# Performance work log

Measured on AMD Instinct MI355X. Metric: run time of the kernel, lower is better.

## Reference

```python
import jax, jax.numpy as jnp
import numpy as np

# Config matching init_kwargs
C, H_IMG, W_IMG = 3, 224, 224
N_PATCHES = 14
PS = H_IMG // N_PATCHES            # 16
INPUT_D = C * PS * PS              # 768
HID = 768
N_HEADS = 12
DH = HID // N_HEADS                # 64
N_BLOCKS = 12
MLP_RATIO = 4
SEQ = N_PATCHES * N_PATCHES + 1    # 197
EPS = 1e-5


def _pos_embed():
    # sin on even dims, cos on odd dims, exponent uses (j - j%2)/d  (faithful to loop)
    i = jnp.arange(SEQ, dtype=jnp.float32)[:, None]
    j = jnp.arange(HID, dtype=jnp.float32)[None, :]
    expo = (j - jnp.mod(j, 2.0)) / HID
    ang = i / jnp.power(10000.0, expo)
    return jnp.where(jnp.mod(jnp.arange(HID), 2) == 0, jnp.sin(ang), jnp.cos(ang))


def setup_inputs() -> dict:
    key = jax.random.key(0)
    ks = jax.random.split(key, 16)
    s = 0.02
    d_ff = MLP_RATIO * HID
    inp = {
        'images': jax.random.normal(ks[0], (16, C, H_IMG, W_IMG), dtype=jnp.float32),
        'w_map': jax.random.normal(ks[1], (HID, INPUT_D), dtype=jnp.float32) * s,
        'b_map': jnp.zeros((HID,), dtype=jnp.float32),
        'class_token': jax.random.uniform(ks[2], (1, HID), dtype=jnp.float32),
        'pos_embed': _pos_embed(),
        'qw': jax.random.normal(ks[3], (N_BLOCKS, N_HEADS, DH, DH), dtype=jnp.float32) * s,
        'qb': jnp.zeros((N_BLOCKS, N_HEADS, DH), dtype=jnp.float32),
        'kw': jax.random.normal(ks[4], (N_BLOCKS, N_HEADS, DH, DH), dtype=jnp.float32) * s,
        'kb': jnp.zeros((N_BLOCKS, N_HEADS, DH), dtype=jnp.float32),
        'vw': jax.random.normal(ks[5], (N_BLOCKS, N_HEADS, DH, DH), dtype=jnp.float32) * s,
        'vb': jnp.zeros((N_BLOCKS, N_HEADS, DH), dtype=jnp.float32),
        'ln1_w': jnp.ones((N_BLOCKS, HID), dtype=jnp.float32),
        'ln1_b': jnp.zeros((N_BLOCKS, HID), dtype=jnp.float32),
        'ln2_w': jnp.ones((N_BLOCKS, HID), dtype=jnp.float32),
        'ln2_b': jnp.zeros((N_BLOCKS, HID), dtype=jnp.float32),
        'mlp_w1': jax.random.normal(ks[6], (N_BLOCKS, d_ff, HID), dtype=jnp.float32) * s,
        'mlp_b1': jnp.zeros((N_BLOCKS, d_ff), dtype=jnp.float32),
        'mlp_w2': jax.random.normal(ks[7], (N_BLOCKS, HID, d_ff), dtype=jnp.float32) * s,
        'mlp_b2': jnp.zeros((N_BLOCKS, HID), dtype=jnp.float32),
    }
    return inp


def _layernorm(x, w, b):
    mu = jnp.mean(x, axis=-1, keepdims=True)
    var = jnp.mean(jnp.square(x - mu), axis=-1, keepdims=True)
    return (x - mu) * jax.lax.rsqrt(var + EPS) * w + b


def _patchify(images):
    # [N,C,H,W] -> [N, np^2, C*ps*ps]; per-patch flatten order is (c, ph, pw)
    n = images.shape[0]
    x = images.reshape(n, C, N_PATCHES, PS, N_PATCHES, PS)
    x = x.transpose(0, 2, 4, 1, 3, 5)  # n, pi, pj, c, ph, pw
    return x.reshape(n, N_PATCHES * N_PATCHES, INPUT_D)


def _msa(x, qw, qb, kw, kb, vw, vb):
    # x: [B,S,D]; per-head Linear on head slices; torch Linear: y = x @ W.T + b
    b_, s_, _ = x.shape
    xh = x.reshape(b_, s_, N_HEADS, DH)
    q = jnp.einsum('bshd,hod->bsho', xh, qw) + qb
    k = jnp.einsum('bshd,hod->bsho', xh, kw) + kb
    v = jnp.einsum('bshd,hod->bsho', xh, vw) + vb
    attn = jax.nn.softmax(jnp.einsum('bsho,btho->bhst', q, k) / (DH ** 0.5), axis=-1)
    out = jnp.einsum('bhst,btho->bsho', attn, v)
    return out.reshape(b_, s_, HID)


def reference(images, w_map, b_map, class_token, pos_embed, qw, qb, kw, kb, vw, vb,
              ln1_w, ln1_b, ln2_w, ln2_b, mlp_w1, mlp_b1, mlp_w2, mlp_b2):
    patches = _patchify(images)                       # [N, 196, 768]
    tokens = patches @ w_map.T + b_map                # [N, 196, HID]
    n = tokens.shape[0]
    cls = jnp.broadcast_to(class_token[None], (n, 1, HID))
    out = jnp.concatenate([cls, tokens], axis=1) + pos_embed[None]  # [N, SEQ, HID]
    for l in range(N_BLOCKS):
        out = out + _msa(_layernorm(out, ln1_w[l], ln1_b[l]),
                         qw[l], qb[l], kw[l], kb[l], vw[l], vb[l])
        h = _layernorm(out, ln2_w[l], ln2_b[l])
        h = jax.nn.gelu(h @ mlp_w1[l].T + mlp_b1[l], approximate=False)
        out = out + (h @ mlp_w2[l].T + mlp_b2[l])
    return out
```

## Files before the change

kernel.cpp:

```cpp
#include <hip/hip_runtime.h>
#include <hip/hip_bf16.h>
#include <math.h>

typedef __attribute__((ext_vector_type(4))) float f32x4;
typedef __attribute__((ext_vector_type(8))) __bf16 bf16x8;
typedef __attribute__((ext_vector_type(8))) short short8;
typedef __attribute__((ext_vector_type(4))) unsigned short us4;
typedef __attribute__((ext_vector_type(8))) unsigned short us8;

#define B_    16
#define SEQ_  197
#define TOK_  3152
#define HID_  768
#define MPAD_ 3200
#define NP_   3136
#define DFF_  3072
#define PSZ_  (MPAD_ * HID_)
#define QKVP_ 14336
#define BHN_  192

__device__ __forceinline__ unsigned short f2bf(float x) {
  union { float f; unsigned int u; } v; v.f = x;
  unsigned int r = v.u + 0x7fffu + ((v.u >> 16) & 1u);
  return (unsigned short)(r >> 16);
}

__device__ __forceinline__ float bf2f(unsigned short u) {
  union { unsigned int i; float f; } v; v.i = ((unsigned int)u) << 16; return v.f;
}

__device__ __forceinline__ f32x4 mfma16(bf16x8 a, bf16x8 b, f32x4 c) {
  return __builtin_amdgcn_mfma_f32_16x16x32_bf16(a, b, c, 0, 0, 0);
}

__device__ __forceinline__ void cp16(const void* g, void* l) {
  __builtin_amdgcn_global_load_lds((__attribute__((address_space(1))) void*)(g),
                                   (__attribute__((address_space(3))) void*)(l),
                                   16, 0, 0);
}

__device__ __forceinline__ float gelu_f(float x) {
  float y = x * (1.5957691216f + 0.0713548162f * x * x);
  float e = __expf(y);
  float r = 1.0f / (1.0f + e);
  return x - x * r;
}

__device__ __forceinline__ void conv8(const float* __restrict__ s, unsigned short* __restrict__ d, int c) {
  const float* sp = s + (size_t)c * 8;
  f32x4 v0 = *(const f32x4*)sp;
  f32x4 v1 = *(const f32x4*)(sp + 4);
  us8 o;
  o[0] = f2bf(v0[0]); o[1] = f2bf(v0[1]); o[2] = f2bf(v0[2]); o[3] = f2bf(v0[3]);
  o[4] = f2bf(v1[0]); o[5] = f2bf(v1[1]); o[6] = f2bf(v1[2]); o[7] = f2bf(v1[3]);
  *(us8*)(d + (size_t)c * 8) = o;
}

__global__ __launch_bounds__(256) void patchcls_kernel(const float* __restrict__ img,
                                                       unsigned short* __restrict__ Pb,
                                                       const float* __restrict__ ct,
                                                       const float* __restrict__ pos,
                                                       float* __restrict__ X,
                                                       const float* __restrict__ wmap,
                                                       unsigned short* __restrict__ Wmb,
                                                       const float* __restrict__ cw1,
                                                       unsigned short* __restrict__ cd1,
                                                       const float* __restrict__ cw2,
                                                       unsigned short* __restrict__ cd2) {
  int bid = blockIdx.x;
  if (bid >= 2736) {
    int bb = bid - 2736;
    const float* s; unsigned short* d;
    if (bb < 1152) { s = cw1; d = cd1; } else { s = cw2; d = cd2; bb -= 1152; }
    conv8(s, d, bb * 256 + threadIdx.x);
    return;
  }
  if (bid >= 2448) {
    int c = (bid - 2448) * 256 + threadIdx.x;
    conv8(wmap, Wmb, c);
    return;
  }
  if (bid >= 2400) {
    int j = (bid - 2400) * 256 + threadIdx.x;
    if (j < B_ * HID_) {
      int b = j / HID_, t = j - b * HID_;
      X[(size_t)b * SEQ_ * HID_ + t] = ct[t] + pos[t];
    }
    return;
  }
  int gid = bid * 256 + threadIdx.x;
  int m = gid / 192;
  int j4 = (gid - m * 192) * 4;
  us4 o;
  if (m < NP_) {
    int n = m / 196, p = m - n * 196;
    int pi = p / 14, pj = p - pi * 14;
    int c = j4 >> 8, rem = j4 & 255, ph = rem >> 4, pw = rem & 15;
    const float* src = img + (((size_t)(n * 3 + c) * 224 + pi * 16 + ph) * 224 + pj * 16 + pw);
    f32x4 v = *(const f32x4*)src;
    o[0] = f2bf(v[0]); o[1] = f2bf(v[1]); o[2] = f2bf(v[2]); o[3] = f2bf(v[3]);
  } else {
    o[0] = 0; o[1] = 0; o[2] = 0; o[3] = 0;
  }
  *(us4*)(Pb + (size_t)m * HID_ + j4) = o;
}

__global__ __launch_bounds__(256) void convw_kernel(const float* __restrict__ s1, unsigned short* __restrict__ d1,
                                                    const float* __restrict__ s2, unsigned short* __restrict__ d2,
                                                    int nchunks) {
  int half = gridDim.x >> 1;
  int b = blockIdx.x;
  const float* s; unsigned short* d;
  if (b < half) { s = s1; d = d1; } else { s = s2; d = d2; b -= half; }
  int c = b * 256 + threadIdx.x;
  if (c >= nchunks) return;
  conv8(s, d, c);
}

__global__ __launch_bounds__(256) void gemm_embed(const unsigned short* __restrict__ A,
                                                  const unsigned short* __restrict__ Bw,
                                                  const float* __restrict__ bias,
                                                  const float* __restrict__ pos,
                                                  float* __restrict__ Xout) {
  constexpr int MI = 2, NJ = 2, BM = 64, BN = 64;
  __shared__ unsigned short As[BM * 64];
  __shared__ unsigned short Bs[BN * 64];
  const int tid = threadIdx.x;
  const int w = tid >> 6, lane = tid & 63;
  const int lr = lane & 15, kg = lane >> 4;
  int bid = blockIdx.x;
  int cpx = gridDim.x >> 3;
  int swz = (bid & 7) * cpx + (bid >> 3);
  const int by = swz / 12, bx = swz - by * 12;
  const int m0 = by * BM, n0 = bx * BN;
  const int wr = w >> 1, wc = w & 1;
  const f32x4 z4 = {0.f, 0.f, 0.f, 0.f};
  f32x4 acc[MI][NJ];
#pragma unroll
  for (int i = 0; i < MI; ++i)
#pragma unroll
    for (int j = 0; j < NJ; ++j) acc[i][j] = z4;
  for (int k0 = 0; k0 < 768; k0 += 64) {
#pragma unroll
    for (int is = 0; is < MI; ++is) {
      int chunk = is * 256 + tid;
      int row = chunk >> 3, cc = (chunk & 7) * 8;
      cp16(A + (size_t)(m0 + row) * 768 + k0 + cc, As + is * 2048 + w * 512);
    }
#pragma unroll
    for (int is = 0; is < NJ; ++is) {
      int chunk = is * 256 + tid;
      int row = chunk >> 3, cc = (chunk & 7) * 8;
      cp16(Bw + (size_t)(n0 + row) * 768 + k0 + cc, Bs + is * 2048 + w * 512);
    }
    __syncthreads();
#pragma unroll
    for (int kk = 0; kk < 64; kk += 32) {
      bf16x8 af[MI], bfr[NJ];
#pragma unroll
      for (int i = 0; i < MI; ++i)
        af[i] = *(const bf16x8*)&As[(wr * (BM / 2) + i * 16 + lr) * 64 + kk + kg * 8];
#pragma unroll
      for (int j = 0; j < NJ; ++j)
        bfr[j] = *(const bf16x8*)&Bs[(wc * (BN / 2) + j * 16 + lr) * 64 + kk + kg * 8];
#pragma unroll
      for (int i = 0; i < MI; ++i)
#pragma unroll
        for (int j = 0; j < NJ; ++j)
          acc[i][j] = mfma16(af[i], bfr[j], acc[i][j]);
    }
    __syncthreads();
  }
#pragma unroll
  for (int i = 0; i < MI; ++i) {
    int mbase = m0 + wr * (BM / 2) + i * 16 + kg * 4;
#pragma unroll
    for (int j = 0; j < NJ; ++j) {
      int col = n0 + wc * (BN / 2) + j * 16 + lr;
#pragma unroll
      for (int qr = 0; qr < 4; ++qr) {
        int m = mbase + qr;
        if (m < NP_) {
          int nimg = m / 196;
          int tok = m + nimg + 1;
          int prow = m - nimg * 196 + 1;
          Xout[(size_t)tok * HID_ + col] = acc[i][j][qr] + bias[col] + pos[(size_t)prow * HID_ + col];
        }
      }
    }
  }
}

template<int EPI, int NT>
__global__ __launch_bounds__(512, 2) void gemm4b(const unsigned short* __restrict__ A,
                                                 const unsigned short* __restrict__ Bw,
                                                 int ldk, int gx, int gy,
                                                 const float* __restrict__ bias,
                                                 unsigned short* __restrict__ Pout,
                                                 unsigned short* __restrict__ Hout) {
  __shared__ unsigned short lds4[32768];
  const int tid = threadIdx.x;
  const int wid = tid >> 6, lane = tid & 63;
  const int lr = lane & 15, kg = lane >> 4;
  const int wm = wid >> 2, wn = wid & 3;
  const int nwg = gridDim.x;
  const int q = nwg >> 3, r = nwg & 7;
  const int xcd = blockIdx.x & 7, idx = blockIdx.x >> 3;
  const int wgid = (xcd < r ? xcd * (q + 1) : r * (q + 1) + (xcd - r) * q) + idx;
  const int bx = wgid % gx;
  const int rest = wgid / gx;
  const int by = rest % gy;
  const int z = rest / gy;
  const int m0 = by * 128, n0 = bx * 128;
  const unsigned short* Abase = A + (size_t)m0 * ldk + z * (NT * 32);
  const unsigned short* Bbase = Bw + (size_t)n0 * ldk + z * (NT * 32);

  const int ra = tid >> 2, ua = tid & 3;
  const int sk = (ua ^ ((ra >> 1) & 3)) * 8;
  const int wbase = wid * 512;

#pragma unroll
  for (int t = 0; t < 3; ++t) {
    unsigned short* lb = lds4 + t * 8192;
    cp16(Abase + (size_t)ra * ldk + sk + t * 32, lb + wbase);
    cp16(Bbase + (size_t)ra * ldk + sk + t * 32, lb + 4096 + wbase);
  }

  int offA[4], offB[2];
#pragma unroll
  for (int i = 0; i < 4; ++i) {
    int rr = wm * 64 + i * 16 + lr;
    offA[i] = rr * 32 + ((kg ^ ((rr >> 1) & 3)) * 8);
  }
#pragma unroll
  for (int j = 0; j < 2; ++j) {
    int rr = wn * 32 + j * 16 + lr;
    offB[j] = rr * 32 + ((kg ^ ((rr >> 1) & 3)) * 8);
  }

  const f32x4 z4 = {0.f, 0.f, 0.f, 0.f};
  f32x4 acc[4][2];
#pragma unroll
  for (int i = 0; i < 4; ++i)
#pragma unroll
    for (int j = 0; j < 2; ++j) acc[i][j] = z4;

#pragma unroll 1
  for (int k = 0; k < NT; ++k) {
    asm volatile("s_waitcnt vmcnt(4)" ::: "memory");
    __builtin_amdgcn_s_barrier();
    __builtin_amdgcn_sched_barrier(0);
    const unsigned short* lp = lds4 + (k & 3) * 8192;
    const int tn = k + 3;
    const int ts = (tn >= NT) ? tn - NT : tn;
    unsigned short* tb = lds4 + (tn & 3) * 8192;
    bf16x8 af[4], bfr[2];
#pragma unroll
    for (int i = 0; i < 4; ++i)
      af[i] = *(const bf16x8*)(lp + offA[i]);
#pragma unroll
    for (int j = 0; j < 2; ++j)
      bfr[j] = *(const bf16x8*)(lp + 4096 + offB[j]);
    cp16(Abase + (size_t)ra * ldk + sk + ts * 32, tb + wbase);
    cp16(Bbase + (size_t)ra * ldk + sk + ts * 32, tb + 4096 + wbase);
    __builtin_amdgcn_s_barrier();
    __builtin_amdgcn_s_setprio(1);
#pragma unroll
    for (int i = 0; i < 4; ++i)
#pragma unroll
      for (int j = 0; j < 2; ++j) acc[i][j] = mfma16(af[i], bfr[j], acc[i][j]);
    __builtin_amdgcn_s_setprio(0);
  }

#pragma unroll
  for (int i = 0; i < 4; ++i) {
    int mbase = m0 + wm * 64 + i * 16 + kg * 4;
#pragma unroll
    for (int j = 0; j < 2; ++j) {
      int col = n0 + wn * 32 + j * 16 + lr;
      float bv = (EPI == 1) ? bias[col] : 0.f;
#pragma unroll
      for (int qr = 0; qr < 4; ++qr) {
        int m = mbase + qr;
        if (m < TOK_) {
          float v = acc[i][j][qr];
          if (EPI == 1) {
            Hout[(size_t)m * 3072 + col] = f2bf(gelu_f(v + bv));
          } else {
            Pout[(size_t)z * PSZ_ + (size_t)m * 768 + col] = f2bf(v);
          }
        }
      }
    }
  }
}

template<int MODE>
__global__ __launch_bounds__(256) void ln_kernel(float* __restrict__ X,
                                                 const unsigned short* __restrict__ P, const float* __restrict__ pb,
                                                 const float* __restrict__ gw, const float* __restrict__ gb,
                                                 unsigned short* __restrict__ Y,
                                                 const float* __restrict__ cw1, unsigned short* __restrict__ cd1,
                                                 const float* __restrict__ cw2, unsigned short* __restrict__ cd2) {
  int bb = (int)blockIdx.x - 800;
  if (bb >= 0) {
    const float* s; unsigned short* d;
    if (bb < 1152) { s = cw1; d = cd1; } else { s = cw2; d = cd2; bb -= 1152; }
    conv8(s, d, bb * 256 + threadIdx.x);
    return;
  }
  int row = blockIdx.x * 4 + (threadIdx.x >> 6);
  int lane = threadIdx.x & 63;
  if (row >= MPAD_) return;
  size_t base = (size_t)row * HID_;
  if (row >= TOK_) {
    us4 zz; zz[0] = 0; zz[1] = 0; zz[2] = 0; zz[3] = 0;
#pragma unroll
    for (int i = 0; i < 3; ++i) *(us4*)(Y + base + i * 256 + lane * 4) = zz;
    return;
  }
  f32x4 xv[3];
  float s1 = 0.f, s2 = 0.f;
#pragma unroll
  for (int i = 0; i < 3; ++i) {
    int cb = i * 256 + lane * 4;
    f32x4 v = *(const f32x4*)(X + base + cb);
    if (MODE == 2) {
      const unsigned short* pp = P + base + cb;
      us4 p0 = *(const us4*)(pp);
      us4 p1 = *(const us4*)(pp + PSZ_);
      us4 p2 = *(const us4*)(pp + 2 * (size_t)PSZ_);
      us4 p3 = *(const us4*)(pp + 3 * (size_t)PSZ_);
      f32x4 bb2 = *(const f32x4*)(pb + cb);
#pragma unroll
      for (int e = 0; e < 4; ++e)
        v[e] += bf2f(p0[e]) + bf2f(p1[e]) + bf2f(p2[e]) + bf2f(p3[e]) + bb2[e];
      *(f32x4*)(X + base + cb) = v;
    }
    xv[i] = v;
    s1 += v[0] + v[1] + v[2] + v[3];
    s2 += v[0] * v[0] + v[1] * v[1] + v[2] * v[2] + v[3] * v[3];
  }
#pragma unroll
  for (int d = 1; d < 64; d <<= 1) {
    s1 += __shfl_xor(s1, d);
    s2 += __shfl_xor(s2, d);
  }
  float mu = s1 * (1.f / 768.f);
  float var = s2 * (1.f / 768.f) - mu * mu;
  float rs = rsqrtf(var + 1e-5f);
#pragma unroll
  for (int i = 0; i < 3; ++i) {
    int cb = i * 256 + lane * 4;
    us4 o;
#pragma unroll
    for (int e = 0; e < 4; ++e)
      o[e] = f2bf((xv[i][e] - mu) * rs * gw[cb + e] + gb[cb + e]);
    *(us4*)(Y + base + cb) = o;
  }
}

__global__ __launch_bounds__(256) void redfin_kernel(float* __restrict__ X, const unsigned short* __restrict__ P,
                                                     const float* __restrict__ b2) {
  int i = blockIdx.x * 256 + threadIdx.x;
  if (i >= TOK_ * 192) return;
  int m = i / 192, c4 = (i - m * 192) * 4;
  size_t off = (size_t)m * HID_ + c4;
  f32x4 v = *(const f32x4*)(X + off);
  const unsigned short* pp = P + off;
  us4 p0 = *(const us4*)(pp);
  us4 p1 = *(const us4*)(pp + PSZ_);
  us4 p2 = *(const us4*)(pp + 2 * (size_t)PSZ_);
  us4 p3 = *(const us4*)(pp + 3 * (size_t)PSZ_);
  f32x4 bb = *(const f32x4*)(b2 + c4);
#pragma unroll
  for (int e = 0; e < 4; ++e)
    v[e] += bf2f(p0[e]) + bf2f(p1[e]) + bf2f(p2[e]) + bf2f(p3[e]) + bb[e];
  *(f32x4*)(X + off) = v;
}

__device__ __forceinline__ void loadw_frags(const float* __restrict__ W, int lr, int kg, bf16x8* wf) {
#pragma unroll
  for (int j = 0; j < 4; ++j)
#pragma unroll
    for (int kk = 0; kk < 2; ++kk) {
      const float* wp = W + (j * 16 + lr) * 64 + kk * 32 + kg * 8;
      f32x4 w0 = *(const f32x4*)wp;
      f32x4 w1 = *(const f32x4*)(wp + 4);
      short8 t;
      t[0] = (short)f2bf(w0[0]); t[1] = (short)f2bf(w0[1]); t[2] = (short)f2bf(w0[2]); t[3] = (short)f2bf(w0[3]);
      t[4] = (short)f2bf(w1[0]); t[5] = (short)f2bf(w1[1]); t[6] = (short)f2bf(w1[2]); t[7] = (short)f2bf(w1[3]);
      wf[j * 2 + kk] = __builtin_bit_cast(bf16x8, t);
    }
}

__global__ __launch_bounds__(128) void qkvproj_kernel(const unsigned short* __restrict__ Y,
                                                      const float* __restrict__ qw, const float* __restrict__ qb,
                                                      const float* __restrict__ kw, const float* __restrict__ kb,
                                                      const float* __restrict__ vw, const float* __restrict__ vb,
                                                      unsigned short* __restrict__ Qo,
                                                      unsigned short* __restrict__ Ko,
                                                      unsigned short* __restrict__ Vto) {
  const int blk = blockIdx.x;
  const int half = blk & 1;
  const int bp = blk >> 1;
  const int p = bp % 3, bh = bp / 3;
  const int b = bh / 12, h = bh - b * 12;
  const int wv = threadIdx.x >> 6, lane = threadIdx.x & 63;
  const int lr = lane & 15, kg = lane >> 4;
  const int ws = half * 2 + wv;
  const float* W; const float* bs; unsigned short* out;
  if (p == 0)      { W = qw + h * 4096; bs = qb + h * 64; out = Qo; }
  else if (p == 1) { W = kw + h * 4096; bs = kb + h * 64; out = Ko; }
  else             { W = vw + h * 4096; bs = vb + h * 64; out = Vto; }
  const float scale = (p == 0) ? 0.125f : 1.0f;
  bf16x8 wf[8];
  loadw_frags(W, lr, kg, wf);
  float bj[4];
#pragma unroll
  for (int j = 0; j < 4; ++j) bj[j] = bs[j * 16 + lr];
  out += (size_t)bh * QKVP_;
  const f32x4 z4 = {0.f, 0.f, 0.f, 0.f};
  const short8 zs = {0, 0, 0, 0, 0, 0, 0, 0};
#pragma unroll
  for (int i = 0; i < 4; ++i) {
    int t = ws + 4 * i;
    if (t < 14) {
      int s = t * 16 + lr;
      bf16x8 a0 = __builtin_bit_cast(bf16x8, zs), a1 = a0;
      if (s < SEQ_) {
        const unsigned short* yp = Y + (size_t)(b * SEQ_ + s) * HID_ + h * 64 + kg * 8;
        a0 = *(const bf16x8*)yp;
        a1 = *(const bf16x8*)(yp + 32);
      }
      f32x4 acc[4] = {z4, z4, z4, z4};
#pragma unroll
      for (int j = 0; j < 4; ++j) {
        acc[j] = mfma16(a0, wf[j * 2 + 0], acc[j]);
        acc[j] = mfma16(a1, wf[j * 2 + 1], acc[j]);
      }
      if (p == 2) {
#pragma unroll
        for (int j = 0; j < 4; ++j) {
          us4 pk;
#pragma unroll
          for (int qr = 0; qr < 4; ++qr) {
            int srow = t * 16 + kg * 4 + qr;
            pk[qr] = (srow < SEQ_) ? f2bf(acc[j][qr] + bj[j]) : (unsigned short)0;
          }
          *(us4*)&out[(j * 16 + lr) * 224 + t * 16 + kg * 4] = pk;
        }
      } else {
#pragma unroll
        for (int j = 0; j < 4; ++j)
#pragma unroll
          for (int qr = 0; qr < 4; ++qr) {
            int row = t * 16 + kg * 4 + qr;
            out[row * 64 + j * 16 + lr] = f2bf((acc[j][qr] + bj[j]) * scale);
          }
      }
    }
  }
}

__global__ __launch_bounds__(64) void attn_kernel(const unsigned short* __restrict__ Qb,
                                                  const unsigned short* __restrict__ Kb,
                                                  const unsigned short* __restrict__ Vtb,
                                                  float* __restrict__ X) {
  __shared__ unsigned short plds[16 * 232];
  const int blk = blockIdx.x;
  const int qt = blk % 13, bh = blk / 13;
  const int b = bh / 12, h = bh - b * 12;
  const int lane = threadIdx.x;
  const int lr = lane & 15, kg = lane >> 4;
  const f32x4 z4 = {0.f, 0.f, 0.f, 0.f};
  const unsigned short* Qp = Qb + (size_t)bh * QKVP_;
  const unsigned short* Kp = Kb + (size_t)bh * QKVP_;
  const unsigned short* Vp = Vtb + (size_t)bh * QKVP_;
  {
    int rr = lane >> 2, c0 = 208 + (lane & 3) * 4;
    us4 zz; zz[0] = 0; zz[1] = 0; zz[2] = 0; zz[3] = 0;
    *(us4*)&plds[rr * 232 + c0] = zz;
  }
  bf16x8 aq0 = *(const bf16x8*)&Qp[(qt * 16 + lr) * 64 + kg * 8];
  bf16x8 aq1 = *(const bf16x8*)&Qp[(qt * 16 + lr) * 64 + 32 + kg * 8];
  f32x4 s[13];
#pragma unroll
  for (int nt = 0; nt < 13; ++nt) {
    const unsigned short* kp = Kp + (nt * 16 + lr) * 64 + kg * 8;
    bf16x8 b0 = *(const bf16x8*)kp;
    bf16x8 b1 = *(const bf16x8*)(kp + 32);
    f32x4 acc = mfma16(aq0, b0, z4);
    s[nt] = mfma16(aq1, b1, acc);
  }
#pragma unroll
  for (int qr = 0; qr < 4; ++qr) {
    float mx = -1e30f;
#pragma unroll
    for (int nt = 0; nt < 13; ++nt) {
      float v = (nt == 12 && lr >= 5) ? -1e30f : s[nt][qr];
      mx = fmaxf(mx, v);
    }
    mx = fmaxf(mx, __shfl_xor(mx, 1));
    mx = fmaxf(mx, __shfl_xor(mx, 2));
    mx = fmaxf(mx, __shfl_xor(mx, 4));
    mx = fmaxf(mx, __shfl_xor(mx, 8));
    float sum = 0.f;
#pragma unroll
    for (int nt = 0; nt < 13; ++nt) {
      float e = (nt == 12 && lr >= 5) ? 0.f : __expf(s[nt][qr] - mx);
      s[nt][qr] = e;
      sum += e;
    }
    sum += __shfl_xor(sum, 1);
    sum += __shfl_xor(sum, 2);
    sum += __shfl_xor(sum, 4);
    sum += __shfl_xor(sum, 8);
    float inv = 1.f / sum;
#pragma unroll
    for (int nt = 0; nt < 13; ++nt)
      plds[(kg * 4 + qr) * 232 + nt * 16 + lr] = f2bf(s[nt][qr] * inv);
  }
  asm volatile("s_waitcnt lgkmcnt(0)" ::: "memory");
  __builtin_amdgcn_sched_barrier(0);
  f32x4 ao[4] = {z4, z4, z4, z4};
#pragma unroll
  for (int kt = 0; kt < 7; ++kt) {
    bf16x8 pa = *(const bf16x8*)&plds[lr * 232 + kt * 32 + kg * 8];
#pragma unroll
    for (int j = 0; j < 4; ++j) {
      bf16x8 bv = *(const bf16x8*)&Vp[(j * 16 + lr) * 224 + kt * 32 + kg * 8];
      ao[j] = mfma16(pa, bv, ao[j]);
    }
  }
#pragma unroll
  for (int j = 0; j < 4; ++j)
#pragma unroll
    for (int qr = 0; qr < 4; ++qr) {
      int ss = qt * 16 + kg * 4 + qr;
      if (ss < SEQ_) {
        size_t xi = (size_t)(b * SEQ_ + ss) * HID_ + h * 64 + j * 16 + lr;
        X[xi] += ao[j][qr];
      }
    }
}

extern "C" void kernel_launch(void* const* d_in, const int* in_sizes, int n_in,
                              void* d_out, int out_size, void* d_ws, size_t ws_size,
                              hipStream_t stream) {
  const float* images = (const float*)d_in[0];
  const float* w_map  = (const float*)d_in[1];
  const float* b_map  = (const float*)d_in[2];
  const float* ctok   = (const float*)d_in[3];
  const float* pos    = (const float*)d_in[4];
  const float* qw   = (const float*)d_in[5];
  const float* qb   = (const float*)d_in[6];
  const float* kw   = (const float*)d_in[7];
  const float* kb   = (const float*)d_in[8];
  const float* vw   = (const float*)d_in[9];
  const float* vb   = (const float*)d_in[10];
  const float* ln1w = (const float*)d_in[11];
  const float* ln1b = (const float*)d_in[12];
  const float* ln2w = (const float*)d_in[13];
  const float* ln2b = (const float*)d_in[14];
  const float* w1   = (const float*)d_in[15];
  const float* b1   = (const float*)d_in[16];
  const float* w2   = (const float*)d_in[17];
  const float* b2   = (const float*)d_in[18];

  float* X = (float*)d_out;

  unsigned short* Y    = (unsigned short*)d_ws;
  unsigned short* Wmb  = Y + (size_t)MPAD_ * HID_;
  unsigned short* Hb   = Wmb + (size_t)768 * 768;
  unsigned short* Pp   = Hb + (size_t)MPAD_ * DFF_;
  unsigned short* Wr   = Pp + 4 * (size_t)PSZ_;

  unsigned short* Qb  = Hb;
  unsigned short* Kb2 = Hb + (size_t)BHN_ * QKVP_;
  unsigned short* Vtb = Hb + 2 * (size_t)BHN_ * QKVP_;

  const size_t L1 = (size_t)DFF_ * HID_;
  const size_t need = ((size_t)MPAD_ * HID_ + (size_t)768 * 768 + (size_t)MPAD_ * DFF_ +
                       4 * (size_t)PSZ_ + 24 * L1) * 2;
  const bool big = ws_size >= need;
  unsigned short* W1r = Wr;
  unsigned short* W2r = Wr + (big ? 12 * L1 : L1);

  patchcls_kernel<<<big ? 5040 : 2736, 256, 0, stream>>>(images, Y, ctok, pos, X,
                                                         w_map, Wmb, w1, W1r, w2, W2r);
  gemm_embed<<<600, 256, 0, stream>>>(Y, Wmb, b_map, pos, X);

  for (int l = 0; l < 12; ++l) {
    unsigned short* W1p = big ? W1r + l * L1 : W1r;
    unsigned short* W2p = big ? W2r + l * L1 : W2r;
    if (l == 0)
      ln_kernel<0><<<800, 256, 0, stream>>>(X, nullptr, nullptr,
                                            ln1w + l * 768, ln1b + l * 768, Y,
                                            nullptr, nullptr, nullptr, nullptr);
    else
      ln_kernel<2><<<800, 256, 0, stream>>>(X, Pp, b2 + (l - 1) * 768,
                                            ln1w + l * 768, ln1b + l * 768, Y,
                                            nullptr, nullptr, nullptr, nullptr);
    qkvproj_kernel<<<1152, 128, 0, stream>>>(Y,
                                             qw + (size_t)l * 49152, qb + l * 768,
                                             kw + (size_t)l * 49152, kb + l * 768,
                                             vw + (size_t)l * 49152, vb + l * 768,
                                             Qb, Kb2, Vtb);
    attn_kernel<<<2496, 64, 0, stream>>>(Qb, Kb2, Vtb, X);
    const bool cvt = big && (l < 11);
    ln_kernel<0><<<cvt ? 3104 : 800, 256, 0, stream>>>(X, nullptr, nullptr,
                                                       ln2w + l * 768, ln2b + l * 768, Y,
                                                       cvt ? w1 + (size_t)(l + 1) * L1 : nullptr,
                                                       cvt ? W1r + (size_t)(l + 1) * L1 : nullptr,
                                                       cvt ? w2 + (size_t)(l + 1) * L1 : nullptr,
                                                       cvt ? W2r + (size_t)(l + 1) * L1 : nullptr);
    if (!big)
      convw_kernel<<<2304, 256, 0, stream>>>(w1 + (size_t)l * L1, W1p,
                                             w2 + (size_t)l * L1, W2p, 294912);
    gemm4b<1, 24><<<600, 512, 0, stream>>>(Y, W1p, 768, 24, 25, b1 + l * 3072, nullptr, Hb);
    gemm4b<3, 24><<<600, 512, 0, stream>>>(Hb, W2p, 3072, 6, 25, nullptr, Pp, nullptr);
  }
  redfin_kernel<<<2364, 256, 0, stream>>>(X, Pp, b2 + 11 * 768);
}
```

Baseline: 1.429 ms.

## Accumulate split-K MLP2 partials into residual with float atomics

The second MLP GEMM no longer writes four bf16 split-K partial buffers that a later LayerNorm or final reduction kernel sums. Each split now atomically adds its fp32 partial straight into the residual stream X, with the bias added by split 0. This removes the partial buffers, the reduce work in the LN kernel and the final redfin kernel, and it also keeps partials in fp32 instead of rounding them to bf16. It costs roughly 4x atomic traffic to X, makes summation order nondeterministic, and drops the second barrier in the GEMM main loop, which may create an LDS race.

```diff
diff --git a/kernel.cpp b/kernel.cpp
--- a/kernel.cpp
+++ b/kernel.cpp
@@ -15,7 +15,6 @@
 #define MPAD_ 3200
 #define NP_   3136
 #define DFF_  3072
-#define PSZ_  (MPAD_ * HID_)
 #define QKVP_ 14336
 #define BHN_  192
 
@@ -196,7 +195,7 @@
                                                  const unsigned short* __restrict__ Bw,
                                                  int ldk, int gx, int gy,
                                                  const float* __restrict__ bias,
-                                                 unsigned short* __restrict__ Pout,
+                                                 float* __restrict__ Xf,
                                                  unsigned short* __restrict__ Hout) {
   __shared__ unsigned short lds4[32768];
   const int tid = threadIdx.x;
@@ -263,7 +262,6 @@
       bfr[j] = *(const bf16x8*)(lp + 4096 + offB[j]);
     cp16(Abase + (size_t)ra * ldk + sk + ts * 32, tb + wbase);
     cp16(Bbase + (size_t)ra * ldk + sk + ts * 32, tb + 4096 + wbase);
-    __builtin_amdgcn_s_barrier();
     __builtin_amdgcn_s_setprio(1);
 #pragma unroll
     for (int i = 0; i < 4; ++i)
@@ -278,16 +276,16 @@
 #pragma unroll
     for (int j = 0; j < 2; ++j) {
       int col = n0 + wn * 32 + j * 16 + lr;
-      float bv = (EPI == 1) ? bias[col] : 0.f;
+      float bv = (EPI == 1 || z == 0) ? bias[col] : 0.f;
 #pragma unroll
       for (int qr = 0; qr < 4; ++qr) {
         int m = mbase + qr;
         if (m < TOK_) {
-          float v = acc[i][j][qr];
+          float v = acc[i][j][qr] + bv;
           if (EPI == 1) {
-            Hout[(size_t)m * 3072 + col] = f2bf(gelu_f(v + bv));
+            Hout[(size_t)m * 3072 + col] = f2bf(gelu_f(v));
           } else {
-            Pout[(size_t)z * PSZ_ + (size_t)m * 768 + col] = f2bf(v);
+            atomicAdd(&Xf[(size_t)m * 768 + col], v);
           }
         }
       }
@@ -295,9 +293,7 @@
   }
 }
 
-template<int MODE>
-__global__ __launch_bounds__(256) void ln_kernel(float* __restrict__ X,
-                                                 const unsigned short* __restrict__ P, const float* __restrict__ pb,
+__global__ __launch_bounds__(256) void ln_kernel(const float* __restrict__ X,
                                                  const float* __restrict__ gw, const float* __restrict__ gb,
                                                  unsigned short* __restrict__ Y,
                                                  const float* __restrict__ cw1, unsigned short* __restrict__ cd1,
@@ -325,18 +321,6 @@
   for (int i = 0; i < 3; ++i) {
     int cb = i * 256 + lane * 4;
     f32x4 v = *(const f32x4*)(X + base + cb);
-    if (MODE == 2) {
-      const unsigned short* pp = P + base + cb;
-      us4 p0 = *(const us4*)(pp);
-      us4 p1 = *(const us4*)(pp + PSZ_);
-      us4 p2 = *(const us4*)(pp + 2 * (size_t)PSZ_);
-      us4 p3 = *(const us4*)(pp + 3 * (size_t)PSZ_);
-      f32x4 bb2 = *(const f32x4*)(pb + cb);
-#pragma unroll
-      for (int e = 0; e < 4; ++e)
-        v[e] += bf2f(p0[e]) + bf2f(p1[e]) + bf2f(p2[e]) + bf2f(p3[e]) + bb2[e];
-      *(f32x4*)(X + base + cb) = v;
-    }
     xv[i] = v;
     s1 += v[0] + v[1] + v[2] + v[3];
     s2 += v[0] * v[0] + v[1] * v[1] + v[2] * v[2] + v[3] * v[3];
@@ -358,25 +342,6 @@
       o[e] = f2bf((xv[i][e] - mu) * rs * gw[cb + e] + gb[cb + e]);
     *(us4*)(Y + base + cb) = o;
   }
-}
-
-__global__ __launch_bounds__(256) void redfin_kernel(float* __restrict__ X, const unsigned short* __restrict__ P,
-                                                     const float* __restrict__ b2) {
-  int i = blockIdx.x * 256 + threadIdx.x;
-  if (i >= TOK_ * 192) return;
-  int m = i / 192, c4 = (i - m * 192) * 4;
-  size_t off = (size_t)m * HID_ + c4;
-  f32x4 v = *(const f32x4*)(X + off);
-  const unsigned short* pp = P + off;
-  us4 p0 = *(const us4*)(pp);
-  us4 p1 = *(const us4*)(pp + PSZ_);
-  us4 p2 = *(const us4*)(pp + 2 * (size_t)PSZ_);
-  us4 p3 = *(const us4*)(pp + 3 * (size_t)PSZ_);
-  f32x4 bb = *(const f32x4*)(b2 + c4);
-#pragma unroll
-  for (int e = 0; e < 4; ++e)
-    v[e] += bf2f(p0[e]) + bf2f(p1[e]) + bf2f(p2[e]) + bf2f(p3[e]) + bb[e];
-  *(f32x4*)(X + off) = v;
 }
 
 __device__ __forceinline__ void loadw_frags(const float* __restrict__ W, int lr, int kg, bf16x8* wf) {
@@ -573,8 +538,7 @@
   unsigned short* Y    = (unsigned short*)d_ws;
   unsigned short* Wmb  = Y + (size_t)MPAD_ * HID_;
   unsigned short* Hb   = Wmb + (size_t)768 * 768;
-  unsigned short* Pp   = Hb + (size_t)MPAD_ * DFF_;
-  unsigned short* Wr   = Pp + 4 * (size_t)PSZ_;
+  unsigned short* Wr   = Hb + (size_t)MPAD_ * DFF_;
 
   unsigned short* Qb  = Hb;
   unsigned short* Kb2 = Hb + (size_t)BHN_ * QKVP_;
@@ -582,7 +546,7 @@
 
   const size_t L1 = (size_t)DFF_ * HID_;
   const size_t need = ((size_t)MPAD_ * HID_ + (size_t)768 * 768 + (size_t)MPAD_ * DFF_ +
-                       4 * (size_t)PSZ_ + 24 * L1) * 2;
+                       24 * L1) * 2;
   const bool big = ws_size >= need;
   unsigned short* W1r = Wr;
   unsigned short* W2r = Wr + (big ? 12 * L1 : L1);
@@ -594,14 +558,8 @@
   for (int l = 0; l < 12; ++l) {
     unsigned short* W1p = big ? W1r + l * L1 : W1r;
     unsigned short* W2p = big ? W2r + l * L1 : W2r;
-    if (l == 0)
-      ln_kernel<0><<<800, 256, 0, stream>>>(X, nullptr, nullptr,
-                                            ln1w + l * 768, ln1b + l * 768, Y,
-                                            nullptr, nullptr, nullptr, nullptr);
-    else
-      ln_kernel<2><<<800, 256, 0, stream>>>(X, Pp, b2 + (l - 1) * 768,
-                                            ln1w + l * 768, ln1b + l * 768, Y,
-                                            nullptr, nullptr, nullptr, nullptr);
+    ln_kernel<<<800, 256, 0, stream>>>(X, ln1w + l * 768, ln1b + l * 768, Y,
+                                       nullptr, nullptr, nullptr, nullptr);
     qkvproj_kernel<<<1152, 128, 0, stream>>>(Y,
                                              qw + (size_t)l * 49152, qb + l * 768,
                                              kw + (size_t)l * 49152, kb + l * 768,
@@ -609,17 +567,15 @@
                                              Qb, Kb2, Vtb);
     attn_kernel<<<2496, 64, 0, stream>>>(Qb, Kb2, Vtb, X);
     const bool cvt = big && (l < 11);
-    ln_kernel<0><<<cvt ? 3104 : 800, 256, 0, stream>>>(X, nullptr, nullptr,
-                                                       ln2w + l * 768, ln2b + l * 768, Y,
-                                                       cvt ? w1 + (size_t)(l + 1) * L1 : nullptr,
-                                                       cvt ? W1r + (size_t)(l + 1) * L1 : nullptr,
-                                                       cvt ? w2 + (size_t)(l + 1) * L1 : nullptr,
-                                                       cvt ? W2r + (size_t)(l + 1) * L1 : nullptr);
+    ln_kernel<<<cvt ? 3104 : 800, 256, 0, stream>>>(X, ln2w + l * 768, ln2b + l * 768, Y,
+                                                    cvt ? w1 + (size_t)(l + 1) * L1 : nullptr,
+                                                    cvt ? W1r + (size_t)(l + 1) * L1 : nullptr,
+                                                    cvt ? w2 + (size_t)(l + 1) * L1 : nullptr,
+                                                    cvt ? W2r + (size_t)(l + 1) * L1 : nullptr);
     if (!big)
       convw_kernel<<<2304, 256, 0, stream>>>(w1 + (size_t)l * L1, W1p,
                                              w2 + (size_t)l * L1, W2p, 294912);
     gemm4b<1, 24><<<600, 512, 0, stream>>>(Y, W1p, 768, 24, 25, b1 + l * 3072, nullptr, Hb);
-    gemm4b<3, 24><<<600, 512, 0, stream>>>(Hb, W2p, 3072, 6, 25, nullptr, Pp, nullptr);
-  }
-  redfin_kernel<<<2364, 256, 0, stream>>>(X, Pp, b2 + 11 * 768);
-}
+    gemm4b<3, 24><<<600, 512, 0, stream>>>(Hb, W2p, 3072, 6, 25, b2 + l * 768, X, nullptr);
+  }
+}
```

After: 1.713 ms. 1.2x slower.

## Fuse LN1 normalization into QKV projection and move weight conversion into up-GEMM

Applied to the files above, without the earlier changes.

The first layernorm now only computes per-row mean and rstd into a small stats buffer, and the QKV projection kernel normalizes fp32 activations on the fly instead of reading a materialized bf16 LN output. This removes one full write and read of the normalized activations per layer. The next layer's MLP weight fp32-to-bf16 conversion blocks move from the LN2 kernel into extra blocks of the up-projection GEMM launch, so they run alongside the GEMM tiles. The GEMM template is split into two specialized kernels with hardcoded tile mapping. The conversion blocks may compete with GEMM tiles for bandwidth, and the QKV kernel now reads fp32 rather than bf16 activations.

```diff
diff --git a/kernel.cpp b/kernel.cpp
--- a/kernel.cpp
+++ b/kernel.cpp
@@ -191,29 +191,35 @@
   }
 }
 
-template<int EPI, int NT>
-__global__ __launch_bounds__(512, 2) void gemm4b(const unsigned short* __restrict__ A,
-                                                 const unsigned short* __restrict__ Bw,
-                                                 int ldk, int gx, int gy,
-                                                 const float* __restrict__ bias,
-                                                 unsigned short* __restrict__ Pout,
-                                                 unsigned short* __restrict__ Hout) {
+__global__ __launch_bounds__(512, 2) void gemm_up(const unsigned short* __restrict__ A,
+                                                  const unsigned short* __restrict__ Bw,
+                                                  const float* __restrict__ bias,
+                                                  unsigned short* __restrict__ Hout,
+                                                  const float* __restrict__ cw1,
+                                                  unsigned short* __restrict__ cd1,
+                                                  const float* __restrict__ cw2,
+                                                  unsigned short* __restrict__ cd2) {
   __shared__ unsigned short lds4[32768];
+  const int bid0 = (int)blockIdx.x;
+  if (bid0 >= 600) {
+    int bb = bid0 - 600;
+    const float* s; unsigned short* d;
+    if (bb < 576) { s = cw1; d = cd1; } else { s = cw2; d = cd2; bb -= 576; }
+    conv8(s, d, bb * 512 + (int)threadIdx.x);
+    return;
+  }
   const int tid = threadIdx.x;
   const int wid = tid >> 6, lane = tid & 63;
   const int lr = lane & 15, kg = lane >> 4;
   const int wm = wid >> 2, wn = wid & 3;
-  const int nwg = gridDim.x;
-  const int q = nwg >> 3, r = nwg & 7;
-  const int xcd = blockIdx.x & 7, idx = blockIdx.x >> 3;
-  const int wgid = (xcd < r ? xcd * (q + 1) : r * (q + 1) + (xcd - r) * q) + idx;
-  const int bx = wgid % gx;
-  const int rest = wgid / gx;
-  const int by = rest % gy;
-  const int z = rest / gy;
+  const int xcd = bid0 & 7, idx = bid0 >> 3;
+  const int wgid = xcd * 75 + idx;
+  const int bx = wgid % 24;
+  const int by = wgid / 24;
   const int m0 = by * 128, n0 = bx * 128;
-  const unsigned short* Abase = A + (size_t)m0 * ldk + z * (NT * 32);
-  const unsigned short* Bbase = Bw + (size_t)n0 * ldk + z * (NT * 32);
+  const int ldk = 768;
+  const unsigned short* Abase = A + (size_t)m0 * ldk;
+  const unsigned short* Bbase = Bw + (size_t)n0 * ldk;
 
   const int ra = tid >> 2, ua = tid & 3;
   const int sk = (ua ^ ((ra >> 1) & 3)) * 8;
@@ -245,6 +251,7 @@
 #pragma unroll
     for (int j = 0; j < 2; ++j) acc[i][j] = z4;
 
+  constexpr int NT = 24;
 #pragma unroll 1
   for (int k = 0; k < NT; ++k) {
     asm volatile("s_waitcnt vmcnt(4)" ::: "memory");
@@ -278,48 +285,119 @@
 #pragma unroll
     for (int j = 0; j < 2; ++j) {
       int col = n0 + wn * 32 + j * 16 + lr;
-      float bv = (EPI == 1) ? bias[col] : 0.f;
+      float bv = bias[col];
 #pragma unroll
       for (int qr = 0; qr < 4; ++qr) {
         int m = mbase + qr;
-        if (m < TOK_) {
-          float v = acc[i][j][qr];
-          if (EPI == 1) {
-            Hout[(size_t)m * 3072 + col] = f2bf(gelu_f(v + bv));
-          } else {
-            Pout[(size_t)z * PSZ_ + (size_t)m * 768 + col] = f2bf(v);
-          }
-        }
+        if (m < TOK_)
+          Hout[(size_t)m * 3072 + col] = f2bf(gelu_f(acc[i][j][qr] + bv));
       }
     }
   }
 }
 
+__global__ __launch_bounds__(512, 2) void gemm_dn(const unsigned short* __restrict__ A,
+                                                  const unsigned short* __restrict__ Bw,
+                                                  unsigned short* __restrict__ Pout) {
+  __shared__ unsigned short lds4[32768];
+  const int tid = threadIdx.x;
+  const int wid = tid >> 6, lane = tid & 63;
+  const int lr = lane & 15, kg = lane >> 4;
+  const int wm = wid >> 2, wn = wid & 3;
+  const int xcd = blockIdx.x & 7, idx = blockIdx.x >> 3;
+  const int wgid = xcd * 75 + idx;
+  const int bx = wgid % 6;
+  const int rest = wgid / 6;
+  const int by = rest % 25;
+  const int z = rest / 25;
+  const int m0 = by * 128, n0 = bx * 128;
+  const int ldk = 3072;
+  constexpr int NT = 24;
+  const unsigned short* Abase = A + (size_t)m0 * ldk + z * (NT * 32);
+  const unsigned short* Bbase = Bw + (size_t)n0 * ldk + z * (NT * 32);
+
+  const int ra = tid >> 2, ua = tid & 3;
+  const int sk = (ua ^ ((ra >> 1) & 3)) * 8;
+  const int wbase = wid * 512;
+
+#pragma unroll
+  for (int t = 0; t < 3; ++t) {
+    unsigned short* lb = lds4 + t * 8192;
+    cp16(Abase + (size_t)ra * ldk + sk + t * 32, lb + wbase);
+    cp16(Bbase + (size_t)ra * ldk + sk + t * 32, lb + 4096 + wbase);
+  }
+
+  int offA[4], offB[2];
+#pragma unroll
+  for (int i = 0; i < 4; ++i) {
+    int rr = wm * 64 + i * 16 + lr;
+    offA[i] = rr * 32 + ((kg ^ ((rr >> 1) & 3)) * 8);
+  }
+#pragma unroll
+  for (int j = 0; j < 2; ++j) {
+    int rr = wn * 32 + j * 16 + lr;
+    offB[j] = rr * 32 + ((kg ^ ((rr >> 1) & 3)) * 8);
+  }
+
+  const f32x4 z4 = {0.f, 0.f, 0.f, 0.f};
+  f32x4 acc[4][2];
+#pragma unroll
+  for (int i = 0; i < 4; ++i)
+#pragma unroll
+    for (int j = 0; j < 2; ++j) acc[i][j] = z4;
+
+#pragma unroll 1
+  for (int k = 0; k < NT; ++k) {
+    asm volatile("s_waitcnt vmcnt(4)" ::: "memory");
+    __builtin_amdgcn_s_barrier();
+    __builtin_amdgcn_sched_barrier(0);
+    const unsigned short* lp = lds4 + (k & 3) * 8192;
+    const int tn = k + 3;
+    const int ts = (tn >= NT) ? tn - NT : tn;
+    unsigned short* tb = lds4 + (tn & 3) * 8192;
+    bf16x8 af[4], bfr[2];
+#pragma unroll
+    for (int i = 0; i < 4; ++i)
+      af[i] = *(const bf16x8*)(lp + offA[i]);
+#pragma unroll
+    for (int j = 0; j < 2; ++j)
+      bfr[j] = *(const bf16x8*)(lp + 4096 + offB[j]);
+    cp16(Abase + (size_t)ra * ldk + sk + ts * 32, tb + wbase);
+    cp16(Bbase + (size_t)ra * ldk + sk + ts * 32, tb + 4096 + wbase);
+    __builtin_amdgcn_s_barrier();
+    __builtin_amdgcn_s_setprio(1);
+#pragma unroll
+    for (int i = 0; i < 4; ++i)
+#pragma unroll
+      for (int j = 0; j < 2; ++j) acc[i][j] = mfma16(af[i], bfr[j], acc[i][j]);
+    __builtin_amdgcn_s_setprio(0);
+  }
+
+#pragma unroll
+  for (int i = 0; i < 4; ++i) {
+    int mbase = m0 + wm * 64 + i * 16 + kg * 4;
+#pragma unroll
+    for (int j = 0; j < 2; ++j) {
+      int col = n0 + wn * 32 + j * 16 + lr;
+#pragma unroll
+      for (int qr = 0; qr < 4; ++qr) {
+        int m = mbase + qr;
+        if (m < TOK_)
+          Pout[(size_t)z * PSZ_ + (size_t)m * 768 + col] = f2bf(acc[i][j][qr]);
+      }
+    }
+  }
+}
+
 template<int MODE>
-__global__ __launch_bounds__(256) void ln_kernel(float* __restrict__ X,
-                                                 const unsigned short* __restrict__ P, const float* __restrict__ pb,
-                                                 const float* __restrict__ gw, const float* __restrict__ gb,
-                                                 unsigned short* __restrict__ Y,
-                                                 const float* __restrict__ cw1, unsigned short* __restrict__ cd1,
-                                                 const float* __restrict__ cw2, unsigned short* __restrict__ cd2) {
-  int bb = (int)blockIdx.x - 800;
-  if (bb >= 0) {
-    const float* s; unsigned short* d;
-    if (bb < 1152) { s = cw1; d = cd1; } else { s = cw2; d = cd2; bb -= 1152; }
-    conv8(s, d, bb * 256 + threadIdx.x);
-    return;
-  }
+__global__ __launch_bounds__(256) void lnstats_kernel(float* __restrict__ X,
+                                                      const unsigned short* __restrict__ P,
+                                                      const float* __restrict__ pb,
+                                                      float* __restrict__ Sb) {
   int row = blockIdx.x * 4 + (threadIdx.x >> 6);
   int lane = threadIdx.x & 63;
-  if (row >= MPAD_) return;
+  if (row >= TOK_) return;
   size_t base = (size_t)row * HID_;
-  if (row >= TOK_) {
-    us4 zz; zz[0] = 0; zz[1] = 0; zz[2] = 0; zz[3] = 0;
-#pragma unroll
-    for (int i = 0; i < 3; ++i) *(us4*)(Y + base + i * 256 + lane * 4) = zz;
-    return;
-  }
-  f32x4 xv[3];
   float s1 = 0.f, s2 = 0.f;
 #pragma unroll
   for (int i = 0; i < 3; ++i) {
@@ -337,6 +415,41 @@
         v[e] += bf2f(p0[e]) + bf2f(p1[e]) + bf2f(p2[e]) + bf2f(p3[e]) + bb2[e];
       *(f32x4*)(X + base + cb) = v;
     }
+    s1 += v[0] + v[1] + v[2] + v[3];
+    s2 += v[0] * v[0] + v[1] * v[1] + v[2] * v[2] + v[3] * v[3];
+  }
+#pragma unroll
+  for (int d = 1; d < 64; d <<= 1) {
+    s1 += __shfl_xor(s1, d);
+    s2 += __shfl_xor(s2, d);
+  }
+  if (lane == 0) {
+    float mu = s1 * (1.f / 768.f);
+    float var = s2 * (1.f / 768.f) - mu * mu;
+    Sb[row * 2] = mu;
+    Sb[row * 2 + 1] = rsqrtf(var + 1e-5f);
+  }
+}
+
+__global__ __launch_bounds__(256) void ln2_kernel(const float* __restrict__ X,
+                                                  const float* __restrict__ gw, const float* __restrict__ gb,
+                                                  unsigned short* __restrict__ Y) {
+  int row = blockIdx.x * 4 + (threadIdx.x >> 6);
+  int lane = threadIdx.x & 63;
+  if (row >= MPAD_) return;
+  size_t base = (size_t)row * HID_;
+  if (row >= TOK_) {
+    us4 zz; zz[0] = 0; zz[1] = 0; zz[2] = 0; zz[3] = 0;
+#pragma unroll
+    for (int i = 0; i < 3; ++i) *(us4*)(Y + base + i * 256 + lane * 4) = zz;
+    return;
+  }
+  f32x4 xv[3];
+  float s1 = 0.f, s2 = 0.f;
+#pragma unroll
+  for (int i = 0; i < 3; ++i) {
+    int cb = i * 256 + lane * 4;
+    f32x4 v = *(const f32x4*)(X + base + cb);
     xv[i] = v;
     s1 += v[0] + v[1] + v[2] + v[3];
     s2 += v[0] * v[0] + v[1] * v[1] + v[2] * v[2] + v[3] * v[3];
@@ -394,7 +507,9 @@
     }
 }
 
-__global__ __launch_bounds__(128) void qkvproj_kernel(const unsigned short* __restrict__ Y,
+__global__ __launch_bounds__(128) void qkvproj_kernel(const float* __restrict__ X,
+                                                      const float* __restrict__ Sb,
+                                                      const float* __restrict__ lw, const float* __restrict__ lb,
                                                       const float* __restrict__ qw, const float* __restrict__ qb,
                                                       const float* __restrict__ kw, const float* __restrict__ kb,
                                                       const float* __restrict__ vw, const float* __restrict__ vb,
@@ -419,6 +534,11 @@
   float bj[4];
 #pragma unroll
   for (int j = 0; j < 4; ++j) bj[j] = bs[j * 16 + lr];
+  const int c0 = h * 64 + kg * 8;
+  f32x4 g0a = *(const f32x4*)(lw + c0),      g0b = *(const f32x4*)(lw + c0 + 4);
+  f32x4 g1a = *(const f32x4*)(lw + c0 + 32), g1b = *(const f32x4*)(lw + c0 + 36);
+  f32x4 e0a = *(const f32x4*)(lb + c0),      e0b = *(const f32x4*)(lb + c0 + 4);
+  f32x4 e1a = *(const f32x4*)(lb + c0 + 32), e1b = *(const f32x4*)(lb + c0 + 36);
   out += (size_t)bh * QKVP_;
   const f32x4 z4 = {0.f, 0.f, 0.f, 0.f};
   const short8 zs = {0, 0, 0, 0, 0, 0, 0, 0};
@@ -429,9 +549,23 @@
       int s = t * 16 + lr;
       bf16x8 a0 = __builtin_bit_cast(bf16x8, zs), a1 = a0;
       if (s < SEQ_) {
-        const unsigned short* yp = Y + (size_t)(b * SEQ_ + s) * HID_ + h * 64 + kg * 8;
-        a0 = *(const bf16x8*)yp;
-        a1 = *(const bf16x8*)(yp + 32);
+        int row = b * SEQ_ + s;
+        const float* xp = X + (size_t)row * HID_ + c0;
+        float mu = Sb[row * 2], rs = Sb[row * 2 + 1];
+        f32x4 x0 = *(const f32x4*)(xp);
+        f32x4 x1 = *(const f32x4*)(xp + 4);
+        f32x4 x2 = *(const f32x4*)(xp + 32);
+        f32x4 x3 = *(const f32x4*)(xp + 36);
+        us8 t0, t1;
+#pragma unroll
+        for (int e = 0; e < 4; ++e) {
+          t0[e]     = f2bf((x0[e] - mu) * rs * g0a[e] + e0a[e]);
+          t0[4 + e] = f2bf((x1[e] - mu) * rs * g0b[e] + e0b[e]);
+          t1[e]     = f2bf((x2[e] - mu) * rs * g1a[e] + e1a[e]);
+          t1[4 + e] = f2bf((x3[e] - mu) * rs * g1b[e] + e1b[e]);
+        }
+        a0 = __builtin_bit_cast(bf16x8, t0);
+        a1 = __builtin_bit_cast(bf16x8, t1);
       }
       f32x4 acc[4] = {z4, z4, z4, z4};
 #pragma unroll
@@ -576,6 +710,8 @@
   unsigned short* Pp   = Hb + (size_t)MPAD_ * DFF_;
   unsigned short* Wr   = Pp + 4 * (size_t)PSZ_;
 
+  float* Sb = (float*)Wmb;
+
   unsigned short* Qb  = Hb;
   unsigned short* Kb2 = Hb + (size_t)BHN_ * QKVP_;
   unsigned short* Vtb = Hb + 2 * (size_t)BHN_ * QKVP_;
@@ -595,31 +731,26 @@
     unsigned short* W1p = big ? W1r + l * L1 : W1r;
     unsigned short* W2p = big ? W2r + l * L1 : W2r;
     if (l == 0)
-      ln_kernel<0><<<800, 256, 0, stream>>>(X, nullptr, nullptr,
-                                            ln1w + l * 768, ln1b + l * 768, Y,
-                                            nullptr, nullptr, nullptr, nullptr);
+      lnstats_kernel<0><<<788, 256, 0, stream>>>(X, nullptr, nullptr, Sb);
     else
-      ln_kernel<2><<<800, 256, 0, stream>>>(X, Pp, b2 + (l - 1) * 768,
-                                            ln1w + l * 768, ln1b + l * 768, Y,
-                                            nullptr, nullptr, nullptr, nullptr);
-    qkvproj_kernel<<<1152, 128, 0, stream>>>(Y,
+      lnstats_kernel<2><<<788, 256, 0, stream>>>(X, Pp, b2 + (l - 1) * 768, Sb);
+    qkvproj_kernel<<<1152, 128, 0, stream>>>(X, Sb, ln1w + l * 768, ln1b + l * 768,
                                              qw + (size_t)l * 49152, qb + l * 768,
                                              kw + (size_t)l * 49152, kb + l * 768,
                                              vw + (size_t)l * 49152, vb + l * 768,
                                              Qb, Kb2, Vtb);
     attn_kernel<<<2496, 64, 0, stream>>>(Qb, Kb2, Vtb, X);
-    const bool cvt = big && (l < 11);
-    ln_kernel<0><<<cvt ? 3104 : 800, 256, 0, stream>>>(X, nullptr, nullptr,
-                                                       ln2w + l * 768, ln2b + l * 768, Y,
-                                                       cvt ? w1 + (size_t)(l + 1) * L1 : nullptr,
-                                                       cvt ? W1r + (size_t)(l + 1) * L1 : nullptr,
-                                                       cvt ? w2 + (size_t)(l + 1) * L1 : nullptr,
-                                                       cvt ? W2r + (size_t)(l + 1) * L1 : nullptr);
+    ln2_kernel<<<800, 256, 0, stream>>>(X, ln2w + l * 768, ln2b + l * 768, Y);
     if (!big)
       convw_kernel<<<2304, 256, 0, stream>>>(w1 + (size_t)l * L1, W1p,
                                              w2 + (size_t)l * L1, W2p, 294912);
-    gemm4b<1, 24><<<600, 512, 0, stream>>>(Y, W1p, 768, 24, 25, b1 + l * 3072, nullptr, Hb);
-    gemm4b<3, 24><<<600, 512, 0, stream>>>(Hb, W2p, 3072, 6, 25, nullptr, Pp, nullptr);
+    const bool cvt = big && (l < 11);
+    gemm_up<<<cvt ? 1752 : 600, 512, 0, stream>>>(Y, W1p, b1 + l * 3072, Hb,
+                                                  cvt ? w1 + (size_t)(l + 1) * L1 : nullptr,
+                                                  cvt ? W1r + (size_t)(l + 1) * L1 : nullptr,
+                                                  cvt ? w2 + (size_t)(l + 1) * L1 : nullptr,
+                                                  cvt ? W2r + (size_t)(l + 1) * L1 : nullptr);
+    gemm_dn<<<600, 512, 0, stream>>>(Hb, W2p, Pp);
   }
   redfin_kernel<<<2364, 256, 0, stream>>>(X, Pp, b2 + 11 * 768);
 }
```

Result: no change. 1.438 ms (+0.7%).
